# Kernel optimization log

Measured on AMD Instinct MI355X. Metric: run time of the kernel, lower is better.

The kernel has to match this reference:

```python
import jax, jax.numpy as jnp
import numpy as np

D_MODEL = 256
N_HEADS = 8
D_K = D_MODEL // N_HEADS
D_HID = D_MODEL // 2
LN_EPS = 1e-5


def setup_inputs() -> dict:
    key = jax.random.key(0)
    ks = jax.random.split(key, 16)
    B, ND, NT = 4, 512, 512
    s = 1.0 / np.sqrt(D_MODEL)
    inp = {
        'detections': jax.random.normal(ks[0], (B, ND, D_MODEL), jnp.float32),
        'tracks': jax.random.normal(ks[1], (B, NT, D_MODEL), jnp.float32),
        # attention projections, torch Linear convention: W [out, in], y = x W^T + b
        'w_q': jax.random.normal(ks[2], (D_MODEL, D_MODEL), jnp.float32) * s,
        'b_q': jnp.zeros((D_MODEL,), jnp.float32),
        'w_k': jax.random.normal(ks[3], (D_MODEL, D_MODEL), jnp.float32) * s,
        'b_k': jnp.zeros((D_MODEL,), jnp.float32),
        'w_v': jax.random.normal(ks[4], (D_MODEL, D_MODEL), jnp.float32) * s,
        'b_v': jnp.zeros((D_MODEL,), jnp.float32),
        'w_o': jax.random.normal(ks[5], (D_MODEL, D_MODEL), jnp.float32) * s,
        'b_o': jnp.zeros((D_MODEL,), jnp.float32),
        # LayerNorm
        'ln_g': jnp.ones((D_MODEL,), jnp.float32),
        'ln_b': jnp.zeros((D_MODEL,), jnp.float32),
        # association head MLP
        'w1': jax.random.normal(ks[6], (D_HID, D_MODEL), jnp.float32) * s,
        'b1': jnp.zeros((D_HID,), jnp.float32),
        'w2': jax.random.normal(ks[7], (1, D_HID), jnp.float32) * (1.0 / np.sqrt(D_HID)),
        'b2': jnp.zeros((1,), jnp.float32),
    }
    return inp


def _forward(detections, tracks, w_q, b_q, w_k, b_k, w_v, b_v, w_o, b_o,
             ln_g, ln_b, w1, b1, w2, b2):
    B, ND, D = detections.shape
    NT = tracks.shape[1]
    # cross-attention: query=detections, key=value=tracks
    Q = (detections @ w_q.T + b_q).reshape(B, ND, N_HEADS, D_K).transpose(0, 2, 1, 3)
    K = (tracks @ w_k.T + b_k).reshape(B, NT, N_HEADS, D_K).transpose(0, 2, 1, 3)
    V = (tracks @ w_v.T + b_v).reshape(B, NT, N_HEADS, D_K).transpose(0, 2, 1, 3)
    scores = jnp.einsum('bhqd,bhkd->bhqk', Q, K) / np.sqrt(D_K)
    attn = jax.nn.softmax(scores, axis=-1)
    ctx = jnp.einsum('bhqk,bhkd->bhqd', attn, V)  # [B,H,ND,D_K]
    ctx = ctx.transpose(0, 2, 1, 3).reshape(B, ND, D)
    attended = ctx @ w_o.T + b_o
    # residual + LayerNorm (dropout = identity in eval)
    x = detections + attended
    mu = jnp.mean(x, axis=-1, keepdims=True)
    var = jnp.var(x, axis=-1, keepdims=True)
    xn = (x - mu) * jax.lax.rsqrt(var + LN_EPS) * ln_g + ln_b
    # pairwise broadcast-multiply + 2-layer MLP + sigmoid
    combined = xn[:, :, None, :] * tracks[:, None, :, :]  # [B,ND,NT,D]
    h = jax.nn.relu(jnp.einsum('bntd,hd->bnth', combined, w1) + b1)
    logits = jnp.einsum('bnth,oh->bnto', h, w2) + b2  # [B,ND,NT,1]
    return jax.nn.sigmoid(logits[..., 0])


def reference(detections, tracks, w_q, b_q, w_k, b_k, w_v, b_v, w_o, b_o,
              ln_g, ln_b, w1, b1, w2, b2):
    return _forward(detections, tracks, w_q, b_q, w_k, b_k, w_v, b_v, w_o, b_o,
                    ln_g, ln_b, w1, b1, w2, b2)
```

## Files before the change

kernel.cpp:

```cpp
#include <hip/hip_runtime.h>

typedef _Float16 half8 __attribute__((ext_vector_type(8)));
typedef _Float16 half4v __attribute__((ext_vector_type(4)));
typedef float f32x4 __attribute__((ext_vector_type(4)));

struct CvtJobs {
    const float* src[7];
    _Float16* dst[7];
    int n[7];
};

__global__ __launch_bounds__(256) void cvt_kernel(CvtJobs j) {
    int job = blockIdx.y;
    const float* s = j.src[job];
    _Float16* d = j.dst[job];
    int n = j.n[job];
    for (int i = blockIdx.x * blockDim.x + threadIdx.x; i < n;
         i += gridDim.x * blockDim.x)
        d[i] = (_Float16)s[i];
}

template<int MODE>
__global__ __launch_bounds__(256) void gemm_tn(
    const _Float16* __restrict__ A, const _Float16* __restrict__ Bm,
    _Float16* __restrict__ Ch, float* __restrict__ Cf,
    const float* __restrict__ bias, float alpha,
    int M, int N, int K, int lda, int ldb, int ldc,
    long oAb, long oAh, long oBb, long oBh, long oCb, long oCh, int ZH)
{
    int z = blockIdx.z;
    int zb = z / ZH, zh = z - zb * ZH;
    A  += zb * oAb + zh * oAh;
    Bm += zb * oBb + zh * oBh;
    long coff = zb * oCb + zh * oCh;

    __shared__ _Float16 As[64][40];
    __shared__ _Float16 Bs[64][40];

    int tid = threadIdx.x;
    int l = tid & 63, w = tid >> 6;
    int wm = (w >> 1) * 32, wn = (w & 1) * 32;
    int m0 = blockIdx.x * 64, n0 = blockIdx.y * 64;
    int lr = tid >> 2, lc = (tid & 3) * 8;
    int ko = (l >> 4) * 8;

    f32x4 acc[2][2]{};

    for (int k0 = 0; k0 < K; k0 += 32) {
        half8 av = *(const half8*)(A + (long)(m0 + lr) * lda + k0 + lc);
        half8 bv{};
        if (n0 + lr < N)
            bv = *(const half8*)(Bm + (long)(n0 + lr) * ldb + k0 + lc);
        __syncthreads();
        *(half8*)(&As[lr][lc]) = av;
        *(half8*)(&Bs[lr][lc]) = bv;
        __syncthreads();
        half8 a0 = *(const half8*)(&As[wm + (l & 15)][ko]);
        half8 a1 = *(const half8*)(&As[wm + 16 + (l & 15)][ko]);
        half8 b0 = *(const half8*)(&Bs[wn + (l & 15)][ko]);
        half8 b1 = *(const half8*)(&Bs[wn + 16 + (l & 15)][ko]);
        acc[0][0] = __builtin_amdgcn_mfma_f32_16x16x32_f16(a0, b0, acc[0][0], 0, 0, 0);
        acc[0][1] = __builtin_amdgcn_mfma_f32_16x16x32_f16(a0, b1, acc[0][1], 0, 0, 0);
        acc[1][0] = __builtin_amdgcn_mfma_f32_16x16x32_f16(a1, b0, acc[1][0], 0, 0, 0);
        acc[1][1] = __builtin_amdgcn_mfma_f32_16x16x32_f16(a1, b1, acc[1][1], 0, 0, 0);
    }

    #pragma unroll
    for (int mm = 0; mm < 2; ++mm)
    #pragma unroll
    for (int nn = 0; nn < 2; ++nn) {
        int row  = wm + mm * 16 + (l >> 4) * 4;
        int colg = n0 + wn + nn * 16 + (l & 15);
        float bc = bias ? bias[colg < N ? colg : 0] : 0.f;
        if (MODE == 2) {
            half4v hv;
            #pragma unroll
            for (int i = 0; i < 4; ++i)
                hv[i] = (_Float16)(acc[mm][nn][i] * alpha + bc);
            int grow = m0 + row;
            int bb = grow >> 9, t = grow & 511;
            long off = ((long)(bb * 8 + (colg >> 5)) * 32 + (colg & 31)) * 512 + t;
            *(half4v*)(Ch + off) = hv;
        } else if (MODE == 0) {
            if (colg < N) {
                #pragma unroll
                for (int i = 0; i < 4; ++i)
                    Ch[coff + (long)(m0 + row + i) * ldc + colg] =
                        (_Float16)(acc[mm][nn][i] * alpha + bc);
            }
        } else {
            if (colg < N) {
                #pragma unroll
                for (int i = 0; i < 4; ++i)
                    Cf[coff + (long)(m0 + row + i) * ldc + colg] =
                        acc[mm][nn][i] * alpha + bc;
            }
        }
    }
}

__global__ __launch_bounds__(512) void softmax_kernel(
    const _Float16* __restrict__ S, _Float16* __restrict__ P)
{
    long base = (long)blockIdx.x * 512;
    int tid = threadIdx.x;
    float v = (float)S[base + tid];
    float m = v;
    #pragma unroll
    for (int off = 32; off; off >>= 1) m = fmaxf(m, __shfl_xor(m, off, 64));
    __shared__ float rm[8], rsum[8];
    int w = tid >> 6;
    if ((tid & 63) == 0) rm[w] = m;
    __syncthreads();
    float mx = rm[0];
    #pragma unroll
    for (int i = 1; i < 8; ++i) mx = fmaxf(mx, rm[i]);
    float e = __expf(v - mx);
    float s = e;
    #pragma unroll
    for (int off = 32; off; off >>= 1) s += __shfl_xor(s, off, 64);
    if ((tid & 63) == 0) rsum[w] = s;
    __syncthreads();
    float tot = rsum[0];
    #pragma unroll
    for (int i = 1; i < 8; ++i) tot += rsum[i];
    P[base + tid] = (_Float16)(e / tot);
}

__global__ __launch_bounds__(256) void ln_kernel(
    const float* __restrict__ det, const float* __restrict__ att,
    const float* __restrict__ g, const float* __restrict__ bta,
    _Float16* __restrict__ xn)
{
    int row = blockIdx.x, tid = threadIdx.x;
    long idx = (long)row * 256 + tid;
    float x = det[idx] + att[idx];
    float s1 = x, s2 = x * x;
    #pragma unroll
    for (int off = 32; off; off >>= 1) {
        s1 += __shfl_xor(s1, off, 64);
        s2 += __shfl_xor(s2, off, 64);
    }
    __shared__ float r1[4], r2[4];
    if ((tid & 63) == 0) { r1[tid >> 6] = s1; r2[tid >> 6] = s2; }
    __syncthreads();
    float S1 = r1[0] + r1[1] + r1[2] + r1[3];
    float S2 = r2[0] + r2[1] + r2[2] + r2[3];
    float mean = S1 * (1.f / 256.f);
    float var  = S2 * (1.f / 256.f) - mean * mean;
    float rs = rsqrtf(var + 1e-5f);
    xn[idx] = (_Float16)((x - mean) * rs * g[tid] + bta[tid]);
}

template<int N_DPP>
__device__ __forceinline__ float dpp_row_ror(float x) {
    return __int_as_float(__builtin_amdgcn_update_dpp(
        0, __float_as_int(x), 0x120 | N_DPP, 0xF, 0xF, true));
}

__global__ __launch_bounds__(256, 2) void mlp_kernel(
    const _Float16* __restrict__ xn, const _Float16* __restrict__ trk,
    const _Float16* __restrict__ w1, const float* __restrict__ w2,
    const float* __restrict__ b1, const float* __restrict__ b2,
    float* __restrict__ out)
{
    int b  = blockIdx.z;
    int n0 = blockIdx.x * 64;
    int t0 = blockIdx.y * 32;
    int tid = threadIdx.x;
    int l = tid & 63, w = tid >> 6;
    int l15 = l & 15, g = l >> 4;
    int ko = g * 8;

    __shared__ _Float16 ts[32][264];
    __shared__ float part[4][32][65];

    {
        const _Float16* src = trk + ((long)b * 512 + t0) * 256;
        int r = tid >> 3, c0 = (tid & 7) * 8;
        #pragma unroll
        for (int c = 0; c < 256; c += 64)
            *(half8*)(&ts[r][c + c0]) = *(const half8*)(src + r * 256 + c + c0);
    }

    int c0 = w * 32 + l15;
    half8 bf[2][8];
    {
        const _Float16* w1p = w1 + c0 * 256 + ko;
        #pragma unroll
        for (int ns = 0; ns < 2; ++ns)
            #pragma unroll
            for (int ks = 0; ks < 8; ++ks)
                bf[ns][ks] = *(const half8*)(w1p + ns * 16 * 256 + ks * 32);
    }
    float w2v0 = w2[c0], w2v1 = w2[c0 + 16];
    float b1v0 = b1[c0], b1v1 = b1[c0 + 16];

    half8 xnf[4][8];
    {
        const _Float16* xb = xn + ((long)b * 512 + n0) * 256 + l15 * 256 + ko;
        #pragma unroll
        for (int m = 0; m < 4; ++m)
            #pragma unroll
            for (int ks = 0; ks < 8; ++ks)
                xnf[m][ks] = *(const half8*)(xb + m * 16 * 256 + ks * 32);
    }

    __syncthreads();

    for (int tl = 0; tl < 32; ++tl) {
        f32x4 acc[4][2]{};
        #pragma unroll
        for (int ks = 0; ks < 8; ++ks) {
            half8 tf = *(const half8*)(&ts[tl][ks * 32 + ko]);
            #pragma unroll
            for (int m = 0; m < 4; ++m) {
                half8 p = xnf[m][ks] * tf;
                acc[m][0] = __builtin_amdgcn_mfma_f32_16x16x32_f16(p, bf[0][ks], acc[m][0], 0, 0, 0);
                acc[m][1] = __builtin_amdgcn_mfma_f32_16x16x32_f16(p, bf[1][ks], acc[m][1], 0, 0, 0);
            }
        }
        #pragma unroll
        for (int m = 0; m < 4; ++m) {
            float v[4];
            #pragma unroll
            for (int i = 0; i < 4; ++i) {
                float h0 = fmaxf(acc[m][0][i] + b1v0, 0.f);
                float h1 = fmaxf(acc[m][1][i] + b1v1, 0.f);
                float x = fmaf(h0, w2v0, h1 * w2v1);
                x += dpp_row_ror<8>(x);
                x += dpp_row_ror<4>(x);
                x += dpp_row_ror<2>(x);
                x += dpp_row_ror<1>(x);
                v[i] = x;
            }
            if (l15 == 0) {
                #pragma unroll
                for (int i = 0; i < 4; ++i)
                    part[w][tl][m * 16 + g * 4 + i] = v[i];
            }
        }
    }
    __syncthreads();

    float b2v = b2[0];
    int t = tid & 31;
    int nbase = tid >> 5;
    float* op = out + ((long)b * 512 + n0) * 512 + t0;
    #pragma unroll
    for (int k = 0; k < 8; ++k) {
        int nn = nbase + k * 8;
        float s = part[0][t][nn] + part[1][t][nn]
                + part[2][t][nn] + part[3][t][nn] + b2v;
        op[(long)nn * 512 + t] = 1.f / (1.f + __expf(-s));
    }
}

extern "C" void kernel_launch(void* const* d_in, const int* in_sizes, int n_in,
                              void* d_out, int out_size, void* d_ws, size_t ws_size,
                              hipStream_t stream)
{
    const float* det  = (const float*)d_in[0];
    const float* trk  = (const float*)d_in[1];
    const float* w_q  = (const float*)d_in[2];
    const float* b_q  = (const float*)d_in[3];
    const float* w_k  = (const float*)d_in[4];
    const float* b_k  = (const float*)d_in[5];
    const float* w_v  = (const float*)d_in[6];
    const float* b_v  = (const float*)d_in[7];
    const float* w_o  = (const float*)d_in[8];
    const float* b_o  = (const float*)d_in[9];
    const float* ln_g = (const float*)d_in[10];
    const float* ln_b = (const float*)d_in[11];
    const float* w1   = (const float*)d_in[12];
    const float* b1   = (const float*)d_in[13];
    const float* w2   = (const float*)d_in[14];
    const float* b2   = (const float*)d_in[15];
    float* out = (float*)d_out;

    char* ws = (char*)d_ws;
    const size_t O_DETH = 0;
    const size_t O_TRKH = O_DETH + (size_t)1048576;
    const size_t O_WQH  = O_TRKH + (size_t)1048576;
    const size_t O_WKH  = O_WQH + 131072;
    const size_t O_WVH  = O_WKH + 131072;
    const size_t O_WOH  = O_WVH + 131072;
    const size_t O_W1H  = O_WOH + 131072;
    const size_t O_QH   = O_W1H + 65536;
    const size_t O_KH   = O_QH + (size_t)1048576;
    const size_t O_VT   = O_KH + (size_t)1048576;
    const size_t O_CTXH = O_VT + (size_t)1048576;
    const size_t O_XNH  = O_CTXH + (size_t)1048576;
    const size_t O_ATT  = O_XNH + (size_t)1048576;
    const size_t O_SC   = O_ATT + (size_t)2097152;
    const size_t O_ATTN = O_SC + (size_t)16777216;

    _Float16* det_h  = (_Float16*)(ws + O_DETH);
    _Float16* trk_h  = (_Float16*)(ws + O_TRKH);
    _Float16* wq_h   = (_Float16*)(ws + O_WQH);
    _Float16* wk_h   = (_Float16*)(ws + O_WKH);
    _Float16* wv_h   = (_Float16*)(ws + O_WVH);
    _Float16* wo_h   = (_Float16*)(ws + O_WOH);
    _Float16* w1_h   = (_Float16*)(ws + O_W1H);
    _Float16* Q_h    = (_Float16*)(ws + O_QH);
    _Float16* K_h    = (_Float16*)(ws + O_KH);
    _Float16* vt     = (_Float16*)(ws + O_VT);
    _Float16* ctx_h  = (_Float16*)(ws + O_CTXH);
    _Float16* xn_h   = (_Float16*)(ws + O_XNH);
    float*    att_f  = (float*)(ws + O_ATT);
    _Float16* sc_h   = (_Float16*)(ws + O_SC);
    _Float16* attn_h = (_Float16*)(ws + O_ATTN);

    CvtJobs cj;
    cj.src[0] = det; cj.dst[0] = det_h; cj.n[0] = 2048 * 256;
    cj.src[1] = trk; cj.dst[1] = trk_h; cj.n[1] = 2048 * 256;
    cj.src[2] = w_q; cj.dst[2] = wq_h;  cj.n[2] = 65536;
    cj.src[3] = w_k; cj.dst[3] = wk_h;  cj.n[3] = 65536;
    cj.src[4] = w_v; cj.dst[4] = wv_h;  cj.n[4] = 65536;
    cj.src[5] = w_o; cj.dst[5] = wo_h;  cj.n[5] = 65536;
    cj.src[6] = w1;  cj.dst[6] = w1_h;  cj.n[6] = 32768;
    cvt_kernel<<<dim3(512, 7), 256, 0, stream>>>(cj);

    gemm_tn<0><<<dim3(32, 4, 1), 256, 0, stream>>>(det_h, wq_h, Q_h, nullptr, b_q, 1.f,
        2048, 256, 256, 256, 256, 256, 0, 0, 0, 0, 0, 0, 1);
    gemm_tn<0><<<dim3(32, 4, 1), 256, 0, stream>>>(trk_h, wk_h, K_h, nullptr, b_k, 1.f,
        2048, 256, 256, 256, 256, 256, 0, 0, 0, 0, 0, 0, 1);
    gemm_tn<2><<<dim3(32, 4, 1), 256, 0, stream>>>(trk_h, wv_h, vt, nullptr, b_v, 1.f,
        2048, 256, 256, 256, 256, 256, 0, 0, 0, 0, 0, 0, 1);
    gemm_tn<0><<<dim3(8, 8, 32), 256, 0, stream>>>(Q_h, K_h, sc_h, nullptr, nullptr,
        0.17677669529663687f,
        512, 512, 32, 256, 256, 512,
        131072, 32, 131072, 32, 2097152, 262144, 8);
    softmax_kernel<<<16384, 512, 0, stream>>>(sc_h, attn_h);
    gemm_tn<0><<<dim3(8, 1, 32), 256, 0, stream>>>(attn_h, vt, ctx_h, nullptr, nullptr, 1.f,
        512, 32, 512, 512, 512, 256,
        2097152, 262144, 131072, 16384, 131072, 32, 8);
    gemm_tn<1><<<dim3(32, 4, 1), 256, 0, stream>>>(ctx_h, wo_h, nullptr, att_f, b_o, 1.f,
        2048, 256, 256, 256, 256, 256, 0, 0, 0, 0, 0, 0, 1);
    ln_kernel<<<2048, 256, 0, stream>>>(det, att_f, ln_g, ln_b, xn_h);
    mlp_kernel<<<dim3(8, 16, 4), 256, 0, stream>>>(xn_h, trk_h, w1_h, w2, b1, b2, out);

    (void)in_sizes; (void)n_in; (void)out_size; (void)ws_size; (void)O_ATTN;
}
```

Measured before the change: 230.0 us.

## Fuse attention into a single flash-style kernel and restructure MLP product

Replaces the separate QK^T GEMM, softmax kernel and PV GEMM with one fused kernel that holds all 512 scores per query in registers, does the softmax in place and multiplies by V through shared memory. This removes the 16 MB fp16 score and probability round trips and two kernel launches. The MLP kernel now multiplies the W1 fragments by the track vector instead of the xn fragments, which cuts the elementwise multiplies per step. It also seeds the accumulators with b1 and reduces the w2 dot product with shuffles instead of DPP. Risks are high register pressure from 32 f32x4 score tiles and the fp16 rounding of the pre-scaled Q.

New measurement: 195.4 us. 1.18x faster.

```diff
diff --git a/kernel.cpp b/kernel.cpp
--- a/kernel.cpp
+++ b/kernel.cpp
@@ -2,6 +2,7 @@
 
 typedef _Float16 half8 __attribute__((ext_vector_type(8)));
 typedef _Float16 half4v __attribute__((ext_vector_type(4)));
+typedef _Float16 half2v __attribute__((ext_vector_type(2)));
 typedef float f32x4 __attribute__((ext_vector_type(4)));
 
 struct CvtJobs {
@@ -25,15 +26,8 @@
     const _Float16* __restrict__ A, const _Float16* __restrict__ Bm,
     _Float16* __restrict__ Ch, float* __restrict__ Cf,
     const float* __restrict__ bias, float alpha,
-    int M, int N, int K, int lda, int ldb, int ldc,
-    long oAb, long oAh, long oBb, long oBh, long oCb, long oCh, int ZH)
-{
-    int z = blockIdx.z;
-    int zb = z / ZH, zh = z - zb * ZH;
-    A  += zb * oAb + zh * oAh;
-    Bm += zb * oBb + zh * oBh;
-    long coff = zb * oCb + zh * oCh;
-
+    int M, int N, int K, int lda, int ldb, int ldc)
+{
     __shared__ _Float16 As[64][40];
     __shared__ _Float16 Bs[64][40];
 
@@ -48,9 +42,7 @@
 
     for (int k0 = 0; k0 < K; k0 += 32) {
         half8 av = *(const half8*)(A + (long)(m0 + lr) * lda + k0 + lc);
-        half8 bv{};
-        if (n0 + lr < N)
-            bv = *(const half8*)(Bm + (long)(n0 + lr) * ldb + k0 + lc);
+        half8 bv = *(const half8*)(Bm + (long)(n0 + lr) * ldb + k0 + lc);
         __syncthreads();
         *(half8*)(&As[lr][lc]) = av;
         *(half8*)(&Bs[lr][lc]) = bv;
@@ -71,7 +63,7 @@
     for (int nn = 0; nn < 2; ++nn) {
         int row  = wm + mm * 16 + (l >> 4) * 4;
         int colg = n0 + wn + nn * 16 + (l & 15);
-        float bc = bias ? bias[colg < N ? colg : 0] : 0.f;
+        float bc = bias ? bias[colg] : 0.f;
         if (MODE == 2) {
             half4v hv;
             #pragma unroll
@@ -82,49 +74,92 @@
             long off = ((long)(bb * 8 + (colg >> 5)) * 32 + (colg & 31)) * 512 + t;
             *(half4v*)(Ch + off) = hv;
         } else if (MODE == 0) {
-            if (colg < N) {
-                #pragma unroll
-                for (int i = 0; i < 4; ++i)
-                    Ch[coff + (long)(m0 + row + i) * ldc + colg] =
-                        (_Float16)(acc[mm][nn][i] * alpha + bc);
-            }
+            #pragma unroll
+            for (int i = 0; i < 4; ++i)
+                Ch[(long)(m0 + row + i) * ldc + colg] =
+                    (_Float16)(acc[mm][nn][i] * alpha + bc);
         } else {
-            if (colg < N) {
-                #pragma unroll
-                for (int i = 0; i < 4; ++i)
-                    Cf[coff + (long)(m0 + row + i) * ldc + colg] =
-                        acc[mm][nn][i] * alpha + bc;
-            }
-        }
-    }
-}
-
-__global__ __launch_bounds__(512) void softmax_kernel(
-    const _Float16* __restrict__ S, _Float16* __restrict__ P)
-{
-    long base = (long)blockIdx.x * 512;
-    int tid = threadIdx.x;
-    float v = (float)S[base + tid];
-    float m = v;
-    #pragma unroll
-    for (int off = 32; off; off >>= 1) m = fmaxf(m, __shfl_xor(m, off, 64));
-    __shared__ float rm[8], rsum[8];
-    int w = tid >> 6;
-    if ((tid & 63) == 0) rm[w] = m;
-    __syncthreads();
-    float mx = rm[0];
-    #pragma unroll
-    for (int i = 1; i < 8; ++i) mx = fmaxf(mx, rm[i]);
-    float e = __expf(v - mx);
-    float s = e;
-    #pragma unroll
-    for (int off = 32; off; off >>= 1) s += __shfl_xor(s, off, 64);
-    if ((tid & 63) == 0) rsum[w] = s;
-    __syncthreads();
-    float tot = rsum[0];
-    #pragma unroll
-    for (int i = 1; i < 8; ++i) tot += rsum[i];
-    P[base + tid] = (_Float16)(e / tot);
+            #pragma unroll
+            for (int i = 0; i < 4; ++i)
+                Cf[(long)(m0 + row + i) * ldc + colg] =
+                    acc[mm][nn][i] * alpha + bc;
+        }
+    }
+}
+
+__global__ __launch_bounds__(256) void flash_kernel(
+    const _Float16* __restrict__ Q, const _Float16* __restrict__ K,
+    const _Float16* __restrict__ vt, _Float16* __restrict__ ctx)
+{
+    __shared__ _Float16 P[4][16][264];
+    int bh = blockIdx.y, b = bh >> 3, h = bh & 7;
+    int q0 = blockIdx.x * 64;
+    int tid = threadIdx.x, l = tid & 63, w = tid >> 6;
+    int l15 = l & 15, g = l >> 4;
+
+    const _Float16* qp = Q + ((long)b * 512 + q0 + w * 16 + l15) * 256 + h * 32 + g * 8;
+    half8 qf = *(const half8*)qp;
+    #pragma unroll
+    for (int i = 0; i < 8; ++i) qf[i] = qf[i] * (_Float16)0.17677669529663687f;
+
+    const _Float16* kp = K + ((long)b * 512 + l15) * 256 + h * 32 + g * 8;
+    f32x4 s[32];
+    f32x4 zero{};
+    #pragma unroll
+    for (int t = 0; t < 32; ++t) {
+        half8 kf = *(const half8*)(kp + (long)t * (16 * 256));
+        s[t] = __builtin_amdgcn_mfma_f32_16x16x32_f16(kf, qf, zero, 0, 0, 0);
+    }
+    float m0 = -3e38f, m1 = -3e38f, m2 = -3e38f, m3 = -3e38f;
+    #pragma unroll
+    for (int t = 0; t < 32; ++t) {
+        m0 = fmaxf(m0, s[t][0]); m1 = fmaxf(m1, s[t][1]);
+        m2 = fmaxf(m2, s[t][2]); m3 = fmaxf(m3, s[t][3]);
+    }
+    float m = fmaxf(fmaxf(m0, m1), fmaxf(m2, m3));
+    m = fmaxf(m, __shfl_xor(m, 16, 64));
+    m = fmaxf(m, __shfl_xor(m, 32, 64));
+    float s0 = 0.f, s1 = 0.f, s2 = 0.f, s3 = 0.f;
+    #pragma unroll
+    for (int t = 0; t < 32; ++t) {
+        s[t][0] = __expf(s[t][0] - m); s0 += s[t][0];
+        s[t][1] = __expf(s[t][1] - m); s1 += s[t][1];
+        s[t][2] = __expf(s[t][2] - m); s2 += s[t][2];
+        s[t][3] = __expf(s[t][3] - m); s3 += s[t][3];
+    }
+    float sum = (s0 + s1) + (s2 + s3);
+    sum += __shfl_xor(sum, 16, 64);
+    sum += __shfl_xor(sum, 32, 64);
+    float rs = 1.f / sum;
+
+    f32x4 c0{}, c1{};
+    const _Float16* vp = vt + ((long)bh * 32 + l15) * 512 + g * 8;
+    #pragma unroll
+    for (int hf = 0; hf < 2; ++hf) {
+        #pragma unroll
+        for (int t = 0; t < 16; ++t) {
+            int tt = hf * 16 + t;
+            half2v p01, p23;
+            p01[0] = (_Float16)s[tt][0]; p01[1] = (_Float16)s[tt][1];
+            p23[0] = (_Float16)s[tt][2]; p23[1] = (_Float16)s[tt][3];
+            *(half2v*)&P[w][l15][t * 16 + g * 4]     = p01;
+            *(half2v*)&P[w][l15][t * 16 + g * 4 + 2] = p23;
+        }
+        #pragma unroll
+        for (int s2i = 0; s2i < 8; ++s2i) {
+            half8 bf = *(const half8*)&P[w][l15][s2i * 32 + g * 8];
+            half8 a0 = *(const half8*)(vp + hf * 256 + s2i * 32);
+            half8 a1 = *(const half8*)(vp + 16 * 512 + hf * 256 + s2i * 32);
+            c0 = __builtin_amdgcn_mfma_f32_16x16x32_f16(a0, bf, c0, 0, 0, 0);
+            c1 = __builtin_amdgcn_mfma_f32_16x16x32_f16(a1, bf, c1, 0, 0, 0);
+        }
+    }
+    _Float16* cp = ctx + ((long)b * 512 + q0 + w * 16 + l15) * 256 + h * 32;
+    #pragma unroll
+    for (int i = 0; i < 4; ++i) {
+        cp[g * 4 + i]      = (_Float16)(c0[i] * rs);
+        cp[16 + g * 4 + i] = (_Float16)(c1[i] * rs);
+    }
 }
 
 __global__ __launch_bounds__(256) void ln_kernel(
@@ -148,14 +183,8 @@
     float S2 = r2[0] + r2[1] + r2[2] + r2[3];
     float mean = S1 * (1.f / 256.f);
     float var  = S2 * (1.f / 256.f) - mean * mean;
-    float rs = rsqrtf(var + 1e-5f);
-    xn[idx] = (_Float16)((x - mean) * rs * g[tid] + bta[tid]);
-}
-
-template<int N_DPP>
-__device__ __forceinline__ float dpp_row_ror(float x) {
-    return __int_as_float(__builtin_amdgcn_update_dpp(
-        0, __float_as_int(x), 0x120 | N_DPP, 0xF, 0xF, true));
+    float rsv = rsqrtf(var + 1e-5f);
+    xn[idx] = (_Float16)((x - mean) * rsv * g[tid] + bta[tid]);
 }
 
 __global__ __launch_bounds__(256, 2) void mlp_kernel(
@@ -183,62 +212,65 @@
             *(half8*)(&ts[r][c + c0]) = *(const half8*)(src + r * 256 + c + c0);
     }
 
-    int c0 = w * 32 + l15;
-    half8 bf[2][8];
+    half8 wf[2][8];
     {
-        const _Float16* w1p = w1 + c0 * 256 + ko;
-        #pragma unroll
-        for (int ns = 0; ns < 2; ++ns)
+        const _Float16* w1p = w1 + (w * 32 + l15) * 256 + ko;
+        #pragma unroll
+        for (int a = 0; a < 2; ++a)
             #pragma unroll
             for (int ks = 0; ks < 8; ++ks)
-                bf[ns][ks] = *(const half8*)(w1p + ns * 16 * 256 + ks * 32);
-    }
-    float w2v0 = w2[c0], w2v1 = w2[c0 + 16];
-    float b1v0 = b1[c0], b1v1 = b1[c0 + 16];
-
-    half8 xnf[4][8];
+                wf[a][ks] = *(const half8*)(w1p + a * 16 * 256 + ks * 32);
+    }
+    f32x4 binit[2]; float w2v[2][4];
+    #pragma unroll
+    for (int a = 0; a < 2; ++a)
+        #pragma unroll
+        for (int i = 0; i < 4; ++i) {
+            int hh = w * 32 + a * 16 + g * 4 + i;
+            binit[a][i] = b1[hh];
+            w2v[a][i]  = w2[hh];
+        }
+
+    half8 bx[4][8];
     {
-        const _Float16* xb = xn + ((long)b * 512 + n0) * 256 + l15 * 256 + ko;
-        #pragma unroll
-        for (int m = 0; m < 4; ++m)
+        const _Float16* xb = xn + ((long)b * 512 + n0 + l15) * 256 + ko;
+        #pragma unroll
+        for (int mm = 0; mm < 4; ++mm)
             #pragma unroll
             for (int ks = 0; ks < 8; ++ks)
-                xnf[m][ks] = *(const half8*)(xb + m * 16 * 256 + ks * 32);
+                bx[mm][ks] = *(const half8*)(xb + mm * 16 * 256 + ks * 32);
     }
 
     __syncthreads();
 
     for (int tl = 0; tl < 32; ++tl) {
-        f32x4 acc[4][2]{};
+        f32x4 acc[2][4];
+        #pragma unroll
+        for (int a = 0; a < 2; ++a)
+            #pragma unroll
+            for (int mm = 0; mm < 4; ++mm) acc[a][mm] = binit[a];
         #pragma unroll
         for (int ks = 0; ks < 8; ++ks) {
             half8 tf = *(const half8*)(&ts[tl][ks * 32 + ko]);
-            #pragma unroll
-            for (int m = 0; m < 4; ++m) {
-                half8 p = xnf[m][ks] * tf;
-                acc[m][0] = __builtin_amdgcn_mfma_f32_16x16x32_f16(p, bf[0][ks], acc[m][0], 0, 0, 0);
-                acc[m][1] = __builtin_amdgcn_mfma_f32_16x16x32_f16(p, bf[1][ks], acc[m][1], 0, 0, 0);
+            half8 sa0 = wf[0][ks] * tf;
+            half8 sa1 = wf[1][ks] * tf;
+            #pragma unroll
+            for (int mm = 0; mm < 4; ++mm) {
+                acc[0][mm] = __builtin_amdgcn_mfma_f32_16x16x32_f16(sa0, bx[mm][ks], acc[0][mm], 0, 0, 0);
+                acc[1][mm] = __builtin_amdgcn_mfma_f32_16x16x32_f16(sa1, bx[mm][ks], acc[1][mm], 0, 0, 0);
             }
         }
         #pragma unroll
-        for (int m = 0; m < 4; ++m) {
-            float v[4];
-            #pragma unroll
-            for (int i = 0; i < 4; ++i) {
-                float h0 = fmaxf(acc[m][0][i] + b1v0, 0.f);
-                float h1 = fmaxf(acc[m][1][i] + b1v1, 0.f);
-                float x = fmaf(h0, w2v0, h1 * w2v1);
-                x += dpp_row_ror<8>(x);
-                x += dpp_row_ror<4>(x);
-                x += dpp_row_ror<2>(x);
-                x += dpp_row_ror<1>(x);
-                v[i] = x;
-            }
-            if (l15 == 0) {
+        for (int mm = 0; mm < 4; ++mm) {
+            float x = 0.f;
+            #pragma unroll
+            for (int a = 0; a < 2; ++a)
                 #pragma unroll
                 for (int i = 0; i < 4; ++i)
-                    part[w][tl][m * 16 + g * 4 + i] = v[i];
-            }
+                    x = fmaf(fmaxf(acc[a][mm][i], 0.f), w2v[a][i], x);
+            x += __shfl_xor(x, 16, 64);
+            x += __shfl_xor(x, 32, 64);
+            if (g == 0) part[w][tl][mm * 16 + l15] = x;
         }
     }
     __syncthreads();
@@ -292,8 +324,6 @@
     const size_t O_CTXH = O_VT + (size_t)1048576;
     const size_t O_XNH  = O_CTXH + (size_t)1048576;
     const size_t O_ATT  = O_XNH + (size_t)1048576;
-    const size_t O_SC   = O_ATT + (size_t)2097152;
-    const size_t O_ATTN = O_SC + (size_t)16777216;
 
     _Float16* det_h  = (_Float16*)(ws + O_DETH);
     _Float16* trk_h  = (_Float16*)(ws + O_TRKH);
@@ -308,8 +338,6 @@
     _Float16* ctx_h  = (_Float16*)(ws + O_CTXH);
     _Float16* xn_h   = (_Float16*)(ws + O_XNH);
     float*    att_f  = (float*)(ws + O_ATT);
-    _Float16* sc_h   = (_Float16*)(ws + O_SC);
-    _Float16* attn_h = (_Float16*)(ws + O_ATTN);
 
     CvtJobs cj;
     cj.src[0] = det; cj.dst[0] = det_h; cj.n[0] = 2048 * 256;
@@ -321,24 +349,17 @@
     cj.src[6] = w1;  cj.dst[6] = w1_h;  cj.n[6] = 32768;
     cvt_kernel<<<dim3(512, 7), 256, 0, stream>>>(cj);
 
-    gemm_tn<0><<<dim3(32, 4, 1), 256, 0, stream>>>(det_h, wq_h, Q_h, nullptr, b_q, 1.f,
-        2048, 256, 256, 256, 256, 256, 0, 0, 0, 0, 0, 0, 1);
-    gemm_tn<0><<<dim3(32, 4, 1), 256, 0, stream>>>(trk_h, wk_h, K_h, nullptr, b_k, 1.f,
-        2048, 256, 256, 256, 256, 256, 0, 0, 0, 0, 0, 0, 1);
-    gemm_tn<2><<<dim3(32, 4, 1), 256, 0, stream>>>(trk_h, wv_h, vt, nullptr, b_v, 1.f,
-        2048, 256, 256, 256, 256, 256, 0, 0, 0, 0, 0, 0, 1);
-    gemm_tn<0><<<dim3(8, 8, 32), 256, 0, stream>>>(Q_h, K_h, sc_h, nullptr, nullptr,
-        0.17677669529663687f,
-        512, 512, 32, 256, 256, 512,
-        131072, 32, 131072, 32, 2097152, 262144, 8);
-    softmax_kernel<<<16384, 512, 0, stream>>>(sc_h, attn_h);
-    gemm_tn<0><<<dim3(8, 1, 32), 256, 0, stream>>>(attn_h, vt, ctx_h, nullptr, nullptr, 1.f,
-        512, 32, 512, 512, 512, 256,
-        2097152, 262144, 131072, 16384, 131072, 32, 8);
-    gemm_tn<1><<<dim3(32, 4, 1), 256, 0, stream>>>(ctx_h, wo_h, nullptr, att_f, b_o, 1.f,
-        2048, 256, 256, 256, 256, 256, 0, 0, 0, 0, 0, 0, 1);
+    gemm_tn<0><<<dim3(32, 4), 256, 0, stream>>>(det_h, wq_h, Q_h, nullptr, b_q, 1.f,
+        2048, 256, 256, 256, 256, 256);
+    gemm_tn<0><<<dim3(32, 4), 256, 0, stream>>>(trk_h, wk_h, K_h, nullptr, b_k, 1.f,
+        2048, 256, 256, 256, 256, 256);
+    gemm_tn<2><<<dim3(32, 4), 256, 0, stream>>>(trk_h, wv_h, vt, nullptr, b_v, 1.f,
+        2048, 256, 256, 256, 256, 256);
+    flash_kernel<<<dim3(8, 32), 256, 0, stream>>>(Q_h, K_h, vt, ctx_h);
+    gemm_tn<1><<<dim3(32, 4), 256, 0, stream>>>(ctx_h, wo_h, nullptr, att_f, b_o, 1.f,
+        2048, 256, 256, 256, 256, 256);
     ln_kernel<<<2048, 256, 0, stream>>>(det, att_f, ln_g, ln_b, xn_h);
     mlp_kernel<<<dim3(8, 16, 4), 256, 0, stream>>>(xn_h, trk_h, w1_h, w2, b1, b2, out);
 
-    (void)in_sizes; (void)n_in; (void)out_size; (void)ws_size; (void)O_ATTN;
-}
+    (void)in_sizes; (void)n_in; (void)out_size; (void)ws_size;
+}
```
